# Kernel optimization log

Measured on AMD Instinct MI355X. Metric: run time of the kernel, lower is better.

## Reference

```python
import jax, jax.numpy as jnp
import numpy as np
from jax import lax

N_SERIES = 1024   # embedding rows
B = 1024          # batch (= rows of Y)
T = 512           # n_time
INPUT = 28        # input_size
OUTPUT = 28       # output_size
N_T = 2           # temporal exogenous channels
N_S = 4           # static features
M = 7             # seasonality[0]


def setup_inputs() -> dict:
    key = jax.random.key(0)
    k1, k2, k3, k4, k5 = jax.random.split(key, 5)
    S = jax.random.normal(k1, (B, N_S), jnp.float32)
    # Y must be strictly positive (division + log in normalize)
    Y = jax.random.uniform(k2, (B, T), jnp.float32, 0.5, 1.5)
    X = jax.random.normal(k3, (B, N_T, T), jnp.float32)
    idxs = jax.random.randint(k4, (B,), 0, N_SERIES)
    sample_mask = jnp.ones((B, T), jnp.float32)
    # embedding table, init near 0.5 like the torch module
    embeds_weight = 0.5 + 0.05 * jax.random.normal(k5, (N_SERIES, 1 + 1 + M), jnp.float32)
    return dict(S=S, Y=Y, X=X, idxs=idxs, sample_mask=sample_mask,
                embeds_weight=embeds_weight)


def _levels_seasons(Y, embeds):
    """Single-seasonality (len(seasonality)==1) ES recurrence via lax.scan."""
    lev_sms = jax.nn.sigmoid(embeds[:, 0])      # [B]
    seas_sms = jax.nn.sigmoid(embeds[:, 1])     # [B]
    init_seas = jnp.exp(embeds[:, 2:2 + M])     # [B, M]
    s0 = init_seas[:, 0]                        # [B]
    lev0 = Y[:, 0] / s0                         # levels[0] = Y0 / seas_prod
    # seasonalities1 list = [s0..s_{M-1}, s0]; step t uses index t, so the
    # rolling buffer of the next M seasonal values starts as [s1..s_{M-1}, s0]
    buf0 = jnp.concatenate([init_seas[:, 1:], s0[:, None]], axis=1)  # [B, M]

    def step(carry, y_t):
        lev, buf = carry
        seas_t = buf[:, 0]
        newlev = lev_sms * (y_t / seas_t) + (1.0 - lev_sms) * lev
        newseas = seas_sms * (y_t / newlev) + (1.0 - seas_sms) * seas_t
        buf = jnp.concatenate([buf[:, 1:], newseas[:, None]], axis=1)
        return (newlev, buf), (newlev, newseas)

    (_, _), (levs, seass) = lax.scan(step, (lev0, buf0), Y[:, 1:].T)  # [T-1, B]
    levels = jnp.concatenate([lev0[:, None], levs.T], axis=1)         # [B, T]
    init_list = jnp.concatenate([init_seas, s0[:, None]], axis=1)     # [B, M+1]
    seasonalities = jnp.concatenate([init_list, seass.T], axis=1)     # [B, T+M]
    return levels, seasonalities


def _forward_core(S, Y, X, idxs, sample_mask, embeds_weight):
    embeds = embeds_weight[idxs]                    # embedding lookup [B, 9]
    levels, seasonalities = _levels_seasons(Y, embeds)

    W = T - INPUT - OUTPUT + 1                      # n_windows
    starts = jnp.arange(W)
    idx_in = starts[:, None] + jnp.arange(INPUT)    # [W, INPUT]

    Yw = Y[:, idx_in]                               # [B, W, INPUT]
    lev_end = levels[:, starts + INPUT - 1]         # [B, W] level at window end
    seas_in = seasonalities[:, idx_in]              # [B, W, INPUT]
    insample = jnp.log(Yw / (lev_end[:, :, None] * seas_in))  # [B, W, INPUT]

    # temporal exogenous: X[:, :, start:end+OUTPUT].reshape(B, -1)
    idx_x = starts[:, None] + jnp.arange(INPUT + OUTPUT)       # [W, I+O]
    Xw = X[:, :, idx_x]                              # [B, N_T, W, I+O]
    Xw = jnp.transpose(Xw, (0, 2, 1, 3)).reshape(Y.shape[0], W, N_T * (INPUT + OUTPUT))
    insample = jnp.concatenate([insample, Xw], axis=2)

    # static features
    Sw = jnp.broadcast_to(S[:, None, :], (Y.shape[0], W, N_S))
    insample = jnp.concatenate([insample, Sw], axis=2)          # [B, W, C]
    windows_y_insample = jnp.transpose(insample, (1, 0, 2))     # [W, B, C]

    # outsample (eval mode: raw Y, not normalized)
    idx_out = starts[:, None] + INPUT + jnp.arange(OUTPUT)      # [W, OUTPUT]
    windows_y_outsample = jnp.transpose(Y[:, idx_out], (1, 0, 2))  # [W, B, O]

    # sample_mask unfold(size=OUTPUT, step=1), keep last W windows
    n_unf = T - OUTPUT + 1
    starts_m = jnp.arange(n_unf)[-W:]
    idx_m = starts_m[:, None] + jnp.arange(OUTPUT)
    mask_w = jnp.transpose(sample_mask[:, idx_m], (1, 0, 2))    # [W, B, O]

    return windows_y_insample, windows_y_outsample, levels, seasonalities, mask_w


def reference(S, Y, X, idxs, sample_mask, embeds_weight):
    return _forward_core(S, Y, X, idxs, sample_mask, embeds_weight)
```

## Files before the change

### kernel.cpp

```cpp
#include <hip/hip_runtime.h>

#define BB   1024
#define TT   512
#define NIN  28
#define NS   4
#define MM   7
#define WW   457
#define SLEN 519
#define EMB  9

#define OUT1_SZ (WW * BB * 144)
#define OUT2_SZ (WW * BB * 28)
#define OUT3_SZ (BB * TT)
#define OUT4_SZ (BB * SLEN)

#define CH   32
#define NCH  (TT / CH)
#define NF1  (WW * BB * 36)
#define NF2  (WW * BB * 7)

typedef float f4 __attribute__((ext_vector_type(4)));

__device__ __forceinline__ f4 ld4u(const float* p) {
    f4 v;
    __builtin_memcpy(&v, p, sizeof(f4));
    return v;
}

__global__ __launch_bounds__(64) void es_scan(const float* __restrict__ Y,
        const int* __restrict__ idxs, const float* __restrict__ EW,
        float* __restrict__ levels, float* __restrict__ seas) {
    __shared__ float yl[64][CH + 1];
    __shared__ float se[64][CH + 1];
    const int tid = threadIdx.x;
    const int b0  = blockIdx.x << 6;
    const int b   = b0 + tid;

    const float* e = EW + idxs[b] * EMB;
    const float lev_sms  = 1.0f / (1.0f + __expf(-e[0]));
    const float seas_sms = 1.0f / (1.0f + __expf(-e[1]));
    const float a_l = 1.0f - lev_sms;
    const float a_s = 1.0f - seas_sms;

    float buf[MM];
    const float is0 = __expf(e[2]);
    {
        float* srow = seas + b * SLEN;
        srow[0] = is0;
#pragma unroll
        for (int k = 1; k < MM; ++k) {
            float v = __expf(e[2 + k]);
            srow[k] = v;
            buf[k - 1] = v;
        }
        buf[MM - 1] = is0;
    }

    f4 pf[8];
#pragma unroll
    for (int k = 0; k < 8; ++k) {
        int flat = (k << 6) + tid;
        int r = flat >> 3, q = flat & 7;
        pf[k] = *reinterpret_cast<const f4*>(Y + (b0 + r) * TT + (q << 2));
    }

    float lev = 0.0f;

#define ES_STEP(TTI)                                                        \
    {                                                                       \
        float y  = yreg[TTI];                                               \
        float st = buf[0];                                                  \
        lev = lev_sms * __fdividef(y, st) + a_l * lev;                      \
        float ns = seas_sms * __fdividef(y, lev) + a_s * st;                \
        buf[0] = buf[1]; buf[1] = buf[2]; buf[2] = buf[3];                  \
        buf[3] = buf[4]; buf[4] = buf[5]; buf[5] = buf[6];                  \
        buf[6] = ns;                                                        \
        yl[tid][TTI] = lev;                                                 \
        se[tid][TTI] = ns;                                                  \
    }

    for (int c = 0; c < NCH; ++c) {
        __syncthreads();
#pragma unroll
        for (int k = 0; k < 8; ++k) {
            int flat = (k << 6) + tid;
            int r = flat >> 3, q = flat & 7;
            float* dst = &yl[r][q << 2];
            dst[0] = pf[k].x; dst[1] = pf[k].y; dst[2] = pf[k].z; dst[3] = pf[k].w;
        }
        __syncthreads();
        if (c < NCH - 1) {
#pragma unroll
            for (int k = 0; k < 8; ++k) {
                int flat = (k << 6) + tid;
                int r = flat >> 3, q = flat & 7;
                pf[k] = *reinterpret_cast<const f4*>(
                    Y + (b0 + r) * TT + (c + 1) * CH + (q << 2));
            }
        }

        float yreg[CH];
#pragma unroll
        for (int tt = 0; tt < CH; ++tt) yreg[tt] = yl[tid][tt];

        if (c == 0) {
            lev = __fdividef(yreg[0], is0);
            yl[tid][0] = lev;
            se[tid][0] = is0;
#pragma unroll
            for (int tt = 1; tt < CH; ++tt) ES_STEP(tt)
        } else {
#pragma unroll
            for (int tt = 0; tt < CH; ++tt) ES_STEP(tt)
        }
        __syncthreads();

#pragma unroll
        for (int k = 0; k < CH; ++k) {
            int flat = (k << 6) + tid;
            int r    = flat >> 5;
            int col  = flat & 31;
            levels[(b0 + r) * TT   + c * CH + col]      = yl[r][col];
            seas  [(b0 + r) * SLEN + MM + c * CH + col] = se[r][col];
        }
    }
#undef ES_STEP
}

__global__ __launch_bounds__(256) void k_pre(const float* __restrict__ levels,
        const float* __restrict__ seas, const float* __restrict__ Y,
        float* __restrict__ LL, float* __restrict__ LYS) {
    int u  = blockIdx.x * 256 + threadIdx.x;
    int b  = u >> 7;
    int t4 = (u & 127) << 2;
    f4 lv = *reinterpret_cast<const f4*>(levels + b * TT + t4);
    f4 yv = *reinterpret_cast<const f4*>(Y      + b * TT + t4);
    f4 sv = ld4u(seas + b * SLEN + t4);
    f4 a, c;
    a.x = __logf(lv.x); a.y = __logf(lv.y); a.z = __logf(lv.z); a.w = __logf(lv.w);
    c.x = __logf(yv.x) - __logf(sv.x);
    c.y = __logf(yv.y) - __logf(sv.y);
    c.z = __logf(yv.z) - __logf(sv.z);
    c.w = __logf(yv.w) - __logf(sv.w);
    *reinterpret_cast<f4*>(LL  + b * TT + t4) = a;
    *reinterpret_cast<f4*>(LYS + b * TT + t4) = c;
}

template<int PRE>
__global__ __launch_bounds__(256) void k_out1_flat(const float* __restrict__ P1,
        const float* __restrict__ P2, const float* __restrict__ Yg,
        const float* __restrict__ X, const float* __restrict__ S,
        f4* __restrict__ out1) {
    int i = blockIdx.x * blockDim.x + threadIdx.x;
    const int stride = gridDim.x * blockDim.x;
    for (; i < NF1; i += stride) {
        int wb  = i / 36;
        int col = i - wb * 36;
        int b   = wb & (BB - 1);
        int w   = wb >> 10;
        f4 v;
        if (col < 7) {
            if (PRE) {
                v = ld4u(P2 + b * TT + w + (col << 2));
                float l = P1[b * TT + w + 27];
                v.x -= l; v.y -= l; v.z -= l; v.w -= l;
            } else {
                int t = w + (col << 2);
                f4 yv = ld4u(Yg + b * TT + t);
                f4 sv = ld4u(P2 + b * SLEN + t);
                float le = P1[b * TT + w + 27];
                v.x = __logf(__fdividef(yv.x, le * sv.x));
                v.y = __logf(__fdividef(yv.y, le * sv.y));
                v.z = __logf(__fdividef(yv.z, le * sv.z));
                v.w = __logf(__fdividef(yv.w, le * sv.w));
            }
        } else if (col < 35) {
            int ch = (col >= 21) ? 1 : 0;
            v = ld4u(X + (size_t)(b * 2 + ch) * TT + w + ((col - 7 - 14 * ch) << 2));
        } else {
            v = *reinterpret_cast<const f4*>(S + (b << 2));
        }
        __builtin_nontemporal_store(v, &out1[i]);
    }
}

__global__ __launch_bounds__(256) void k_out25(const float* __restrict__ Y,
        const float* __restrict__ mask, f4* __restrict__ out2,
        f4* __restrict__ out5) {
    int i = blockIdx.x * blockDim.x + threadIdx.x;
    const int stride = gridDim.x * blockDim.x;
    for (; i < NF2; i += stride) {
        int wb = i / 7;
        int j  = i - wb * 7;
        int b  = wb & (BB - 1);
        int w  = wb >> 10;
        int base = w + NIN + (j << 2);
        f4 vy = ld4u(Y    + b * TT + base);
        f4 vm = ld4u(mask + b * TT + base);
        __builtin_nontemporal_store(vy, &out2[i]);
        __builtin_nontemporal_store(vm, &out5[i]);
    }
}

extern "C" void kernel_launch(void* const* d_in, const int* in_sizes, int n_in,
                              void* d_out, int out_size, void* d_ws, size_t ws_size,
                              hipStream_t stream) {
    const float* S    = (const float*)d_in[0];
    const float* Y    = (const float*)d_in[1];
    const float* X    = (const float*)d_in[2];
    const int*   idxs = (const int*)d_in[3];
    const float* mask = (const float*)d_in[4];
    const float* EW   = (const float*)d_in[5];

    float* out  = (float*)d_out;
    float* out1 = out;
    float* out2 = out1 + OUT1_SZ;
    float* out3 = out2 + OUT2_SZ;
    float* out4 = out3 + OUT3_SZ;
    float* out5 = out4 + OUT4_SZ;

    es_scan<<<16, 64, 0, stream>>>(Y, idxs, EW, out3, out4);

    const size_t need = (size_t)2 * BB * TT * sizeof(float);
    if (ws_size >= need) {
        float* LL  = (float*)d_ws;
        float* LYS = LL + BB * TT;
        k_pre<<<512, 256, 0, stream>>>(out3, out4, Y, LL, LYS);
        k_out1_flat<1><<<2048, 256, 0, stream>>>(LL, LYS, Y, X, S, (f4*)out1);
    } else {
        k_out1_flat<0><<<2048, 256, 0, stream>>>(out3, out4, Y, X, S, (f4*)out1);
    }
    k_out25<<<2048, 256, 0, stream>>>(Y, mask, (f4*)out2, (f4*)out5);
}
```

Baseline: 117.4 us.

## Fuse log precompute into ES scan and make out1 gather branchless

The log(level) and log(y)-log(seas) precompute moves into the serial ES scan kernel, which now writes both workspace arrays directly, so the separate k_pre launch and its global re-read go away. The out1 kernel becomes branchless: per-column source pointers and strides sit in a shared-memory table, non-level columns subtract a zero read from workspace, and each thread handles two elements per iteration. The tradeoff is extra transcendental work and shared-memory traffic inside the 16-block scan, which is latency bound and may lengthen the critical path.

```diff
diff --git a/kernel.cpp b/kernel.cpp
--- a/kernel.cpp
+++ b/kernel.cpp
@@ -20,6 +20,7 @@
 #define NF2  (WW * BB * 7)
 
 typedef float f4 __attribute__((ext_vector_type(4)));
+typedef unsigned long long u64;
 
 __device__ __forceinline__ f4 ld4u(const float* p) {
     f4 v;
@@ -27,11 +28,16 @@
     return v;
 }
 
+template<int WRITE_WS>
 __global__ __launch_bounds__(64) void es_scan(const float* __restrict__ Y,
         const int* __restrict__ idxs, const float* __restrict__ EW,
-        float* __restrict__ levels, float* __restrict__ seas) {
+        float* __restrict__ levels, float* __restrict__ seas,
+        float* __restrict__ LLg, float* __restrict__ LYSg,
+        float* __restrict__ Wz) {
     __shared__ float yl[64][CH + 1];
     __shared__ float se[64][CH + 1];
+    __shared__ float llb[64][CH + 1];
+    __shared__ float lyb[64][CH + 1];
     const int tid = threadIdx.x;
     const int b0  = blockIdx.x << 6;
     const int b   = b0 + tid;
@@ -77,6 +83,10 @@
         buf[6] = ns;                                                        \
         yl[tid][TTI] = lev;                                                 \
         se[tid][TTI] = ns;                                                  \
+        if (WRITE_WS) {                                                     \
+            llb[tid][TTI] = __logf(lev);                                    \
+            lyb[tid][TTI] = __logf(y) - __logf(st);                         \
+        }                                                                   \
     }
 
     for (int c = 0; c < NCH; ++c) {
@@ -107,6 +117,10 @@
             lev = __fdividef(yreg[0], is0);
             yl[tid][0] = lev;
             se[tid][0] = is0;
+            if (WRITE_WS) {
+                llb[tid][0] = __logf(lev);
+                lyb[tid][0] = __logf(yreg[0]) - __logf(is0);
+            }
 #pragma unroll
             for (int tt = 1; tt < CH; ++tt) ES_STEP(tt)
         } else {
@@ -122,33 +136,83 @@
             int col  = flat & 31;
             levels[(b0 + r) * TT   + c * CH + col]      = yl[r][col];
             seas  [(b0 + r) * SLEN + MM + c * CH + col] = se[r][col];
+            if (WRITE_WS) {
+                LLg [(b0 + r) * TT + c * CH + col] = llb[r][col];
+                LYSg[(b0 + r) * TT + c * CH + col] = lyb[r][col];
+            }
         }
     }
 #undef ES_STEP
-}
-
-__global__ __launch_bounds__(256) void k_pre(const float* __restrict__ levels,
-        const float* __restrict__ seas, const float* __restrict__ Y,
-        float* __restrict__ LL, float* __restrict__ LYS) {
-    int u  = blockIdx.x * 256 + threadIdx.x;
-    int b  = u >> 7;
-    int t4 = (u & 127) << 2;
-    f4 lv = *reinterpret_cast<const f4*>(levels + b * TT + t4);
-    f4 yv = *reinterpret_cast<const f4*>(Y      + b * TT + t4);
-    f4 sv = ld4u(seas + b * SLEN + t4);
-    f4 a, c;
-    a.x = __logf(lv.x); a.y = __logf(lv.y); a.z = __logf(lv.z); a.w = __logf(lv.w);
-    c.x = __logf(yv.x) - __logf(sv.x);
-    c.y = __logf(yv.y) - __logf(sv.y);
-    c.z = __logf(yv.z) - __logf(sv.z);
-    c.w = __logf(yv.w) - __logf(sv.w);
-    *reinterpret_cast<f4*>(LL  + b * TT + t4) = a;
-    *reinterpret_cast<f4*>(LYS + b * TT + t4) = c;
-}
-
-template<int PRE>
-__global__ __launch_bounds__(256) void k_out1_flat(const float* __restrict__ P1,
-        const float* __restrict__ P2, const float* __restrict__ Yg,
+    if (WRITE_WS && blockIdx.x == 0 && tid == 0) Wz[0] = 0.0f;
+}
+
+__global__ __launch_bounds__(256) void k_out1_bl(const float* __restrict__ LL,
+        const float* __restrict__ LYS, const float* __restrict__ Wz,
+        const float* __restrict__ X, const float* __restrict__ S,
+        f4* __restrict__ out1) {
+    __shared__ u64 tp[36];
+    __shared__ u64 tlp[36];
+    __shared__ int4 ts4[36];
+
+    const int tid = threadIdx.x;
+    if (tid < 36) {
+        const int col = tid;
+        u64 p, lp; int4 s;
+        if (col < 7) {
+            p  = (u64)(uintptr_t)(LYS + (col << 2));
+            lp = (u64)(uintptr_t)(LL + 27);
+            s  = make_int4(TT, 1, TT, 1);
+        } else if (col < 21) {
+            p  = (u64)(uintptr_t)(X + ((col - 7) << 2));
+            lp = (u64)(uintptr_t)Wz;
+            s  = make_int4(2 * TT, 1, 0, 0);
+        } else if (col < 35) {
+            p  = (u64)(uintptr_t)(X + TT + ((col - 21) << 2));
+            lp = (u64)(uintptr_t)Wz;
+            s  = make_int4(2 * TT, 1, 0, 0);
+        } else {
+            p  = (u64)(uintptr_t)S;
+            lp = (u64)(uintptr_t)Wz;
+            s  = make_int4(NS, 0, 0, 0);
+        }
+        tp[col] = p; tlp[col] = lp; ts4[col] = s;
+    }
+    __syncthreads();
+
+    const int stride = gridDim.x * blockDim.x;
+    int i = blockIdx.x * blockDim.x + tid;
+
+#define BODY(I, A, L)                                                       \
+    {                                                                       \
+        int wb  = (I) / 36;                                                 \
+        int col = (I) - wb * 36;                                            \
+        int b   = wb & (BB - 1);                                            \
+        int w   = wb >> 10;                                                 \
+        int4 s  = ts4[col];                                                 \
+        const float* src  = (const float*)(uintptr_t)tp[col]  + b * s.x + w * s.y; \
+        const float* lsrc = (const float*)(uintptr_t)tlp[col] + b * s.z + w * s.w; \
+        A = ld4u(src);                                                      \
+        L = *lsrc;                                                          \
+    }
+
+    for (; i < NF1; i += 2 * stride) {
+        int i2 = i + stride;
+        f4 a1, a2; float l1, l2;
+        BODY(i, a1, l1)
+        bool ok2 = (i2 < NF1);
+        if (ok2) BODY(i2, a2, l2)
+        f4 v1; v1.x = a1.x - l1; v1.y = a1.y - l1; v1.z = a1.z - l1; v1.w = a1.w - l1;
+        __builtin_nontemporal_store(v1, &out1[i]);
+        if (ok2) {
+            f4 v2; v2.x = a2.x - l2; v2.y = a2.y - l2; v2.z = a2.z - l2; v2.w = a2.w - l2;
+            __builtin_nontemporal_store(v2, &out1[i2]);
+        }
+    }
+#undef BODY
+}
+
+__global__ __launch_bounds__(256) void k_out1_flat0(const float* __restrict__ levels,
+        const float* __restrict__ seas, const float* __restrict__ Yg,
         const float* __restrict__ X, const float* __restrict__ S,
         f4* __restrict__ out1) {
     int i = blockIdx.x * blockDim.x + threadIdx.x;
@@ -160,20 +224,14 @@
         int w   = wb >> 10;
         f4 v;
         if (col < 7) {
-            if (PRE) {
-                v = ld4u(P2 + b * TT + w + (col << 2));
-                float l = P1[b * TT + w + 27];
-                v.x -= l; v.y -= l; v.z -= l; v.w -= l;
-            } else {
-                int t = w + (col << 2);
-                f4 yv = ld4u(Yg + b * TT + t);
-                f4 sv = ld4u(P2 + b * SLEN + t);
-                float le = P1[b * TT + w + 27];
-                v.x = __logf(__fdividef(yv.x, le * sv.x));
-                v.y = __logf(__fdividef(yv.y, le * sv.y));
-                v.z = __logf(__fdividef(yv.z, le * sv.z));
-                v.w = __logf(__fdividef(yv.w, le * sv.w));
-            }
+            int t = w + (col << 2);
+            f4 yv = ld4u(Yg + b * TT + t);
+            f4 sv = ld4u(seas + b * SLEN + t);
+            float le = levels[b * TT + w + 27];
+            v.x = __logf(__fdividef(yv.x, le * sv.x));
+            v.y = __logf(__fdividef(yv.y, le * sv.y));
+            v.z = __logf(__fdividef(yv.z, le * sv.z));
+            v.w = __logf(__fdividef(yv.w, le * sv.w));
         } else if (col < 35) {
             int ch = (col >= 21) ? 1 : 0;
             v = ld4u(X + (size_t)(b * 2 + ch) * TT + w + ((col - 7 - 14 * ch) << 2));
@@ -219,16 +277,17 @@
     float* out4 = out3 + OUT3_SZ;
     float* out5 = out4 + OUT4_SZ;
 
-    es_scan<<<16, 64, 0, stream>>>(Y, idxs, EW, out3, out4);
-
-    const size_t need = (size_t)2 * BB * TT * sizeof(float);
+    const size_t need = ((size_t)2 * BB * TT + 1) * sizeof(float);
     if (ws_size >= need) {
         float* LL  = (float*)d_ws;
         float* LYS = LL + BB * TT;
-        k_pre<<<512, 256, 0, stream>>>(out3, out4, Y, LL, LYS);
-        k_out1_flat<1><<<2048, 256, 0, stream>>>(LL, LYS, Y, X, S, (f4*)out1);
+        float* Wz  = LYS + BB * TT;
+        es_scan<1><<<16, 64, 0, stream>>>(Y, idxs, EW, out3, out4, LL, LYS, Wz);
+        k_out1_bl<<<2048, 256, 0, stream>>>(LL, LYS, Wz, X, S, (f4*)out1);
     } else {
-        k_out1_flat<0><<<2048, 256, 0, stream>>>(out3, out4, Y, X, S, (f4*)out1);
+        es_scan<0><<<16, 64, 0, stream>>>(Y, idxs, EW, out3, out4,
+                                          nullptr, nullptr, nullptr);
+        k_out1_flat0<<<2048, 256, 0, stream>>>(out3, out4, Y, X, S, (f4*)out1);
     }
     k_out25<<<2048, 256, 0, stream>>>(Y, mask, (f4*)out2, (f4*)out5);
 }
```

After: 202.1 us. 72.2% more time.
